# Kernel tuning notes

Measured on AMD Instinct MI355X. Metric: run time of the kernel, lower is better.

Reference implementation:

```python
import jax, jax.numpy as jnp
import numpy as np
import math

DIM = 1024
N_HEADS = 16
HEAD_DIM = DIM // N_HEADS
MAX_SEQ_LEN = 2048


def rope_tables(seq_len, head_dim):
    inv_freq = 1.0 / (10000.0 ** (jnp.arange(0, head_dim, 2, dtype=jnp.float32) / head_dim))
    t = jnp.arange(seq_len, dtype=jnp.float32)
    freqs = jnp.einsum('i,j->ij', t, inv_freq)          # [T, D/2]
    emb = jnp.concatenate([freqs, freqs], axis=-1)      # [T, D]
    return jnp.cos(emb), jnp.sin(emb)


def rotate_half(x):
    x1, x2 = jnp.split(x, 2, axis=-1)
    return jnp.concatenate([-x2, x1], axis=-1)


def setup_inputs() -> dict:
    key = jax.random.key(0)
    k1, k2, k3 = jax.random.split(key, 3)
    B, T = 4, 2048
    x = jax.random.normal(k1, (B, T, DIM), dtype=jnp.float32)
    # Linear(dim, 3*dim, bias=False) and Linear(dim, dim, bias=False); stored as [in, out]
    Wqkv = jax.random.normal(k2, (DIM, 3 * DIM), dtype=jnp.float32) * (1.0 / math.sqrt(DIM))
    Wproj = jax.random.normal(k3, (DIM, DIM), dtype=jnp.float32) * (1.0 / math.sqrt(DIM))
    return {"x": x, "Wqkv": Wqkv, "Wproj": Wproj}


def reference(x, Wqkv, Wproj):
    B, T, C = x.shape
    qkv = x @ Wqkv                                       # [B,T,3C]
    q, k, v = jnp.split(qkv, 3, axis=-1)
    # [B,T,C] -> [B,H,T,D]
    def to_heads(t_):
        return t_.reshape(B, T, N_HEADS, HEAD_DIM).transpose(0, 2, 1, 3)
    q, k, v = to_heads(q), to_heads(k), to_heads(v)
    cos, sin = rope_tables(T, HEAD_DIM)                  # [T,D]
    cos = cos[None, None, :, :]
    sin = sin[None, None, :, :]
    q = q * cos + rotate_half(q) * sin
    k = k * cos + rotate_half(k) * sin
    scale = 1.0 / math.sqrt(HEAD_DIM)
    att = jnp.einsum('bhqd,bhkd->bhqk', q, k) * scale    # [B,H,T,T]
    causal = jnp.triu(jnp.ones((T, T), dtype=bool), k=1)
    att = jnp.where(causal[None, None], -jnp.inf, att)
    att = jax.nn.softmax(att, axis=-1)
    y = jnp.einsum('bhqk,bhkd->bhqd', att, v)            # [B,H,T,D]
    y = y.transpose(0, 2, 1, 3).reshape(B, T, C)
    return y @ Wproj
```

## Files before the change

### kernel.cpp

```cpp
#include <hip/hip_runtime.h>
#include <hip/hip_bf16.h>

typedef unsigned short u16;
typedef __attribute__((ext_vector_type(8))) short short8;
typedef __attribute__((ext_vector_type(4))) float floatx4;

__device__ __forceinline__ u16 f2bf(float f) {
    union { float f; unsigned u; } v; v.f = f;
    unsigned r = v.u + 0x7fffu + ((v.u >> 16) & 1u);
    return (u16)(r >> 16);
}
__device__ __forceinline__ float fexp2(float x) {
#if __has_builtin(__builtin_amdgcn_exp2f)
    return __builtin_amdgcn_exp2f(x);
#else
    return exp2f(x);
#endif
}
__device__ __forceinline__ unsigned cvtpk_bf16(float lo, float hi) {
    unsigned r;
    asm("v_cvt_pk_bf16_f32 %0, %1, %2" : "=v"(r) : "v"(lo), "v"(hi));
    return r;
}
__device__ __forceinline__ void permlane32_swap(unsigned &a, unsigned &b) {
    asm("v_permlane32_swap_b32 %0, %1" : "+v"(a), "+v"(b));
}
__device__ __forceinline__ void permlane16_swap(unsigned &a, unsigned &b) {
    asm("v_permlane16_swap_b32 %0, %1" : "+v"(a), "+v"(b));
}

__device__ __forceinline__ void async_load16(const void* g, void* l) {
    __builtin_amdgcn_global_load_lds(
        (const __attribute__((address_space(1))) unsigned int*)g,
        (__attribute__((address_space(3))) unsigned int*)l, 16, 0, 0);
}

#define B_   4
#define T_   2048
#define NH_  16
#define HD_  64
#define DIM_ 1024
#define M_   (B_ * T_)
#define NQKV (3 * DIM_)
#define NT_  16
#define LOG2E 1.4426950408889634f

__global__ __launch_bounds__(256) void preproc(const float* __restrict__ x,
                                               const float* __restrict__ Wqkv,
                                               const float* __restrict__ Wproj,
                                               u16* __restrict__ xb,
                                               u16* __restrict__ wqt,
                                               u16* __restrict__ wpt,
                                               float* __restrict__ tabc,
                                               float* __restrict__ tabs) {
    __shared__ float tile[32][33];
    const int bid = blockIdx.x, tid = threadIdx.x;
    if (bid < 8192) {
        int idx = bid * 256 + tid;
        float4 v = ((const float4*)x)[idx];
        ushort4 o;
        o.x = f2bf(v.x); o.y = f2bf(v.y); o.z = f2bf(v.z); o.w = f2bf(v.w);
        ((ushort4*)xb)[idx] = o;
    } else if (bid < 12288) {
        const float* in; u16* outp; int Cn, bx, by;
        if (bid < 11264) { int blk = bid - 8192;  in = Wqkv;  outp = wqt; Cn = NQKV; bx = blk % 96; by = blk / 96; }
        else             { int blk = bid - 11264; in = Wproj; outp = wpt; Cn = DIM_; bx = blk & 31; by = blk >> 5; }
        const int R = DIM_;
        int c0 = bx * 32, r0 = by * 32;
        int tx = tid & 31, ty = tid >> 5;
#pragma unroll
        for (int i = 0; i < 4; ++i)
            tile[ty + i * 8][tx] = in[(size_t)(r0 + ty + i * 8) * Cn + c0 + tx];
        __syncthreads();
#pragma unroll
        for (int i = 0; i < 4; ++i)
            outp[(size_t)(c0 + ty + i * 8) * R + r0 + tx] = f2bf(tile[tx][ty + i * 8]);
    } else {
        int idx = (bid - 12288) * 256 + tid;
        int t = idx >> 5, j = idx & 31;
        double invf = pow(10000.0, -(double)j / 32.0);
        double th = (double)t * invf;
        tabc[idx] = (float)cos(th);
        tabs[idx] = (float)sin(th);
    }
}

__device__ __forceinline__ void gemm_core(const u16* __restrict__ A,
                                          const u16* __restrict__ Bt,
                                          u16* smem, int m0, int n0, int tid,
                                          floatx4 (&acc)[2][4]) {
    const int wave = tid >> 6, lane = tid & 63;
    const int ln15 = lane & 15, quad = lane >> 4;
    const int wm = (wave & 3) * 32, wn = (wave >> 2) * 64;
    const int l8 = lane & 7, ld8 = lane >> 3;
    const int sgc = (l8 ^ ld8) * 8;
    const int K = DIM_;

    const u16* aS = A + (size_t)(m0 + wave * 8 + ld8) * K + sgc;
    const u16* bS = Bt + (size_t)(n0 + wave * 16 + ld8) * K + sgc;

    auto issue3 = [&](int k2, u16* As2, u16* Bs2) {
        async_load16(aS + k2,          As2 + (wave * 8) * 64);
        async_load16(bS + k2,          Bs2 + (wave * 16) * 64);
        async_load16(bS + 8 * K + k2,  Bs2 + (wave * 16 + 8) * 64);
    };
    auto compute = [&](const u16* As_c, const u16* Bs_c, int c4) {
        short8 af[2], bfv[4];
#pragma unroll
        for (int i = 0; i < 2; ++i) {
            int row = wm + i * 16 + ln15;
            af[i] = *(const short8*)&As_c[row * 64 + (((c4 + quad) ^ (row & 7)) << 3)];
        }
#pragma unroll
        for (int j = 0; j < 4; ++j) {
            int row = wn + j * 16 + ln15;
            bfv[j] = *(const short8*)&Bs_c[row * 64 + (((c4 + quad) ^ (row & 7)) << 3)];
        }
        __builtin_amdgcn_s_setprio(1);
#pragma unroll
        for (int i = 0; i < 2; ++i)
#pragma unroll
            for (int j = 0; j < 4; ++j)
                acc[i][j] = __builtin_amdgcn_mfma_f32_16x16x32_bf16(
                    af[i], bfv[j], acc[i][j], 0, 0, 0);
        __builtin_amdgcn_s_setprio(0);
    };

    issue3(0, smem, smem + 24576);
    issue3(64, smem + 8192, smem + 24576 + 16384);

#pragma unroll 1
    for (int t = 0; t < NT_; ++t) {
        if (t < NT_ - 1) asm volatile("s_waitcnt vmcnt(3)" ::: "memory");
        else             asm volatile("s_waitcnt vmcnt(0)" ::: "memory");
        __builtin_amdgcn_s_barrier();
        asm volatile("" ::: "memory");

        const int cb = t % 3, cb2 = (t + 2) % 3;
        const u16* As_c = smem + cb * 8192;
        const u16* Bs_c = smem + 24576 + cb * 16384;
        u16* As2 = smem + cb2 * 8192;
        u16* Bs2 = smem + 24576 + cb2 * 16384;

        if (t < NT_ - 2) issue3((t + 2) * 64, As2, Bs2);
        compute(As_c, Bs_c, 0);
        compute(As_c, Bs_c, 4);
        asm volatile("" ::: "memory");
    }
}

__global__ __launch_bounds__(1024, 4) void gemm_qkv(const u16* __restrict__ A,
                                                    const u16* __restrict__ Bt,
                                                    const float* __restrict__ tabc,
                                                    const float* __restrict__ tabs,
                                                    u16* __restrict__ Qo,
                                                    u16* __restrict__ Ko,
                                                    u16* __restrict__ Vt) {
    __shared__ __align__(16) u16 smem[73728];
    const int tid = threadIdx.x;
    const int bid = blockIdx.x;
    const int wg = (bid & 7) * 96 + (bid >> 3);
    const int bx = wg / 64, by = wg - bx * 64;
    const int m0 = by * 128, n0 = bx * 256;

    floatx4 acc[2][4] = {};
    gemm_core(A, Bt, smem, m0, n0, tid, acc);

    const int wave = tid >> 6, lane = tid & 63;
    const int ln15 = lane & 15, quad = lane >> 4;
    const int wm = (wave & 3) * 32, wn = (wave >> 2) * 64;

    __syncthreads();
    u16* Es = smem;
    const int sel = n0 >> 10;
    auto es_put = [&](int row, int col, u16 v) {
        int c = col >> 3;
        int pc = (c & 24) | ((c & 7) ^ (row & 7));
        Es[row * 256 + pc * 8 + (col & 7)] = v;
    };
    if (sel == 2) {
#pragma unroll
        for (int i = 0; i < 2; ++i)
#pragma unroll
            for (int j = 0; j < 4; ++j)
#pragma unroll
                for (int r = 0; r < 4; ++r)
                    es_put(wm + i * 16 + quad * 4 + r, wn + j * 16 + ln15,
                           f2bf(acc[i][j][r]));
    } else {
        const float scale = sel ? 1.0f : 0.125f * LOG2E;
#pragma unroll
        for (int i = 0; i < 2; ++i)
#pragma unroll
            for (int jjl = 0; jjl < 2; ++jjl) {
                int j = jjl * 16 + ln15;
#pragma unroll
                for (int r = 0; r < 4; ++r) {
                    int row = wm + i * 16 + quad * 4 + r;
                    int t = (m0 + row) & (T_ - 1);
                    float cs = tabc[t * 32 + j], sn = tabs[t * 32 + j];
                    float xl = acc[i][jjl][r], xh = acc[i][jjl + 2][r];
                    es_put(row, wn + j,      f2bf((xl * cs - xh * sn) * scale));
                    es_put(row, wn + j + 32, f2bf((xh * cs + xl * sn) * scale));
                }
            }
    }
    __syncthreads();
    if (sel == 2) {
        const int bq = m0 >> 11;
        const int t0 = m0 & (T_ - 1);
        const int h0 = (n0 & 1023) >> 6;
#pragma unroll
        for (int a = 0; a < 2; ++a) {
            int aid = tid + a * 1024;
            int hh = aid >> 9;
            int rem = aid & 511;
            int tseg = rem >> 5;
            int d2 = rem & 31;
            int col = hh * 64 + 2 * d2;
            int cch = col >> 3;
            u16 lo8[8], hi8[8];
#pragma unroll
            for (int j = 0; j < 8; ++j) {
                int row = tseg * 8 + j;
                int pc = (cch & 24) | ((cch & 7) ^ (row & 7));
                unsigned w = *(const unsigned*)&Es[row * 256 + pc * 8 + (col & 7)];
                lo8[j] = (u16)(w & 0xffffu);
                hi8[j] = (u16)(w >> 16);
            }
            size_t ob = ((size_t)((bq * NH_ + h0 + hh) * HD_) + 2 * d2) * T_ + t0 + tseg * 8;
            *(uint4*)(Vt + ob) = *(const uint4*)lo8;
            *(uint4*)(Vt + ob + T_) = *(const uint4*)hi8;
        }
    } else {
        const int bb = m0 >> 11;
        u16* outqk = (sel == 1) ? Ko : Qo;
#pragma unroll
        for (int k = 0; k < 4; ++k) {
            int cid = tid + k * 1024;
            int row = cid >> 5, c = cid & 31;
            int pc = (c & 24) | ((c & 7) ^ (row & 7));
            uint4 v = *(const uint4*)&Es[row * 256 + pc * 8];
            int h = ((n0 & 1023) >> 6) + (c >> 3);
            int d = (c & 7) * 8;
            int t = (m0 + row) & (T_ - 1);
            *(uint4*)&outqk[((size_t)(bb * NH_ + h) * T_ + t) * HD_ + d] = v;
        }
    }
}

__device__ __forceinline__ void gemm_core128(const u16* __restrict__ A,
                                             const u16* __restrict__ Bt,
                                             u16* smem, int m0, int n0, int tid,
                                             floatx4 (&acc)[4][4]) {
    const int wave = tid >> 6, lane = tid & 63;
    const int ln15 = lane & 15, quad = lane >> 4;
    const int wm = (wave & 1) * 64, wn = (wave >> 1) * 64;
    const int l8 = lane & 7, ld8 = lane >> 3;
    const int sgc = (l8 ^ ld8) * 8;
    const int K = DIM_;

    const u16* aS = A + (size_t)(m0 + wave * 32 + ld8) * K + sgc;
    const u16* bS = Bt + (size_t)(n0 + wave * 32 + ld8) * K + sgc;

    auto stage = [&](int k0, u16* buf) {
#pragma unroll
        for (int it = 0; it < 4; ++it) {
            async_load16(aS + (size_t)(it * 8) * K + k0,
                         buf + (wave * 32 + it * 8) * 64);
            async_load16(bS + (size_t)(it * 8) * K + k0,
                         buf + 8192 + (wave * 32 + it * 8) * 64);
        }
    };
    auto compute = [&](const u16* buf, int c4) {
        short8 af[4], bfv[4];
#pragma unroll
        for (int i = 0; i < 4; ++i) {
            int row = wm + i * 16 + ln15;
            af[i] = *(const short8*)&buf[row * 64 + (((c4 + quad) ^ (row & 7)) << 3)];
        }
#pragma unroll
        for (int j = 0; j < 4; ++j) {
            int row = wn + j * 16 + ln15;
            bfv[j] = *(const short8*)&buf[8192 + row * 64 + (((c4 + quad) ^ (row & 7)) << 3)];
        }
        __builtin_amdgcn_s_setprio(1);
#pragma unroll
        for (int i = 0; i < 4; ++i)
#pragma unroll
            for (int j = 0; j < 4; ++j)
                acc[i][j] = __builtin_amdgcn_mfma_f32_16x16x32_bf16(
                    af[i], bfv[j], acc[i][j], 0, 0, 0);
        __builtin_amdgcn_s_setprio(0);
    };

    stage(0, smem);
#pragma unroll 1
    for (int t = 0; t < NT_; ++t) {
        asm volatile("s_waitcnt vmcnt(0)" ::: "memory");
        __builtin_amdgcn_s_barrier();
        asm volatile("" ::: "memory");
        if (t + 1 < NT_) stage((t + 1) * 64, smem + ((t + 1) & 1) * 16384);
        const u16* cur = smem + (t & 1) * 16384;
        compute(cur, 0);
        compute(cur, 4);
        asm volatile("" ::: "memory");
    }
}

__global__ __launch_bounds__(256, 4) void gemm_proj(const u16* __restrict__ A,
                                                    const u16* __restrict__ Bt,
                                                    float* __restrict__ C) {
    __shared__ __align__(16) u16 smem[32768];
    const int tid = threadIdx.x;
    const int bid = blockIdx.x;
    const int local = bid >> 3;
    const int by = (bid & 7) * 8 + (local & 7);
    const int bx = local >> 3;
    const int m0 = by * 128, n0 = bx * 128;

    floatx4 acc[4][4] = {};
    gemm_core128(A, Bt, smem, m0, n0, tid, acc);

    const int wave = tid >> 6, lane = tid & 63;
    const int ln15 = lane & 15, quad = lane >> 4;
    const int wm = (wave & 1) * 64, wn = (wave >> 1) * 64;
#pragma unroll
    for (int i = 0; i < 4; ++i)
#pragma unroll
        for (int jj = 0; jj < 4; ++jj)
#pragma unroll
            for (int r = 0; r < 4; ++r) {
                int m = m0 + wm + i * 16 + quad * 4 + r;
                int n = n0 + wn + jj * 16 + ln15;
                C[(size_t)m * DIM_ + n] = acc[i][jj][r];
            }
}

__global__ __launch_bounds__(256, 5) void attn_kernel(const u16* __restrict__ Q,
                                                      const u16* __restrict__ Kh,
                                                      const u16* __restrict__ Vt,
                                                      u16* __restrict__ Y) {
    __shared__ __align__(16) u16 Kl[2][64 * 64];
    __shared__ __align__(16) u16 Vl[2][64 * 64];
    const int tid = threadIdx.x, wave = tid >> 6, lane = tid & 63;
    const int ln15 = lane & 15, quad = lane >> 4;
    const int bid = blockIdx.x;
    const int tidx = 31 - (bid >> 6);
    const int bh = bid & 63;
    const int b = bh >> 4, h = bh & 15;
    const int l8 = lane & 7, ld8 = lane >> 3;
    const int sgc = l8 ^ ld8;

    const u16* kbase = Kh + (size_t)bh * T_ * HD_;
    const u16* vbase = Vt + (size_t)bh * HD_ * T_;
    const short8 ones = {0x3F80, 0x3F80, 0x3F80, 0x3F80,
                         0x3F80, 0x3F80, 0x3F80, 0x3F80};
    const int srow = wave * 16;

    const int q0 = tidx * 64;
    const int bm = q0 + srow;

    const u16* qp = Q + ((size_t)bh * T_ + bm + ln15) * HD_;
    short8 qf0 = *(const short8*)(qp + quad * 8);
    short8 qf1 = *(const short8*)(qp + 32 + quad * 8);

    floatx4 o[5] = {};

#pragma unroll
    for (int it = 0; it < 2; ++it) {
        int r = srow + it * 8;
        async_load16(kbase + (size_t)(r + ld8) * HD_ + sgc * 8, &Kl[0][r * 64]);
        async_load16(vbase + (size_t)(r + ld8) * T_ + sgc * 8, &Vl[0][r * 64]);
    }

    for (int kt = 0; kt <= tidx; ++kt) {
        const int cur = kt & 1;
        __syncthreads();
        if (kt < tidx) {
            const int kn = (kt + 1) * 64;
#pragma unroll
            for (int it = 0; it < 2; ++it) {
                int r = srow + it * 8;
                async_load16(kbase + (size_t)(kn + r + ld8) * HD_ + sgc * 8,
                             &Kl[cur ^ 1][r * 64]);
                async_load16(vbase + (size_t)(r + ld8) * T_ + kn + sgc * 8,
                             &Vl[cur ^ 1][r * 64]);
            }
        }
        floatx4 s[4] = {};
        __builtin_amdgcn_s_setprio(1);
#pragma unroll
        for (int nt = 0; nt < 4; ++nt) {
            int row = nt * 16 + ln15;
            short8 kf0 = *(const short8*)&Kl[cur][row * 64 + ((quad ^ (row & 7)) << 3)];
            short8 kf1 = *(const short8*)&Kl[cur][row * 64 + (((4 + quad) ^ (row & 7)) << 3)];
            s[nt] = __builtin_amdgcn_mfma_f32_16x16x32_bf16(kf0, qf0, s[nt], 0, 0, 0);
            s[nt] = __builtin_amdgcn_mfma_f32_16x16x32_bf16(kf1, qf1, s[nt], 0, 0, 0);
        }
        __builtin_amdgcn_s_setprio(0);
        if (kt == tidx) {
            const int lim = srow + ln15;
#pragma unroll
            for (int nt = 0; nt < 4; ++nt) {
                int key = nt * 16 + quad * 4;
#pragma unroll
                for (int r = 0; r < 4; ++r)
                    s[nt][r] = (key + r > lim) ? 0.f : fexp2(s[nt][r]);
            }
        } else {
#pragma unroll
            for (int nt = 0; nt < 4; ++nt)
#pragma unroll
                for (int r = 0; r < 4; ++r) s[nt][r] = fexp2(s[nt][r]);
        }
        unsigned x0 = cvtpk_bf16(s[0][0], s[0][1]);
        unsigned x1 = cvtpk_bf16(s[1][0], s[1][1]);
        unsigned y0 = cvtpk_bf16(s[0][2], s[0][3]);
        unsigned y1 = cvtpk_bf16(s[1][2], s[1][3]);
        unsigned x2 = cvtpk_bf16(s[2][0], s[2][1]);
        unsigned x3 = cvtpk_bf16(s[3][0], s[3][1]);
        unsigned y2 = cvtpk_bf16(s[2][2], s[2][3]);
        unsigned y3 = cvtpk_bf16(s[3][2], s[3][3]);
        permlane32_swap(x0, x1); permlane16_swap(x0, x1);
        permlane32_swap(y0, y1); permlane16_swap(y0, y1);
        permlane32_swap(x2, x3); permlane16_swap(x2, x3);
        permlane32_swap(y2, y3); permlane16_swap(y2, y3);
        union { unsigned u[4]; short8 s8; } pk0, pk1;
        pk0.u[0] = x0; pk0.u[1] = y0; pk0.u[2] = x1; pk0.u[3] = y1;
        pk1.u[0] = x2; pk1.u[1] = y2; pk1.u[2] = x3; pk1.u[3] = y3;
        __builtin_amdgcn_s_setprio(1);
#pragma unroll
        for (int nt = 0; nt < 4; ++nt) {
            int row = nt * 16 + ln15;
            short8 vf0 = *(const short8*)&Vl[cur][row * 64 + ((quad ^ (row & 7)) << 3)];
            short8 vf1 = *(const short8*)&Vl[cur][row * 64 + (((4 + quad) ^ (row & 7)) << 3)];
            o[nt] = __builtin_amdgcn_mfma_f32_16x16x32_bf16(pk0.s8, vf0, o[nt], 0, 0, 0);
            o[nt] = __builtin_amdgcn_mfma_f32_16x16x32_bf16(pk1.s8, vf1, o[nt], 0, 0, 0);
        }
        o[4] = __builtin_amdgcn_mfma_f32_16x16x32_bf16(pk0.s8, ones, o[4], 0, 0, 0);
        o[4] = __builtin_amdgcn_mfma_f32_16x16x32_bf16(pk1.s8, ones, o[4], 0, 0, 0);
        __builtin_amdgcn_s_setprio(0);
    }
#pragma unroll
    for (int r = 0; r < 4; ++r) {
        float inv = 1.f / o[4][r];
        int row = bm + quad * 4 + r;
        u16* yp = Y + ((size_t)(b * T_ + row)) * DIM_ + h * HD_;
#pragma unroll
        for (int nt = 0; nt < 4; ++nt)
            yp[nt * 16 + ln15] = f2bf(o[nt][r] * inv);
    }
}

extern "C" void kernel_launch(void* const* d_in, const int* in_sizes, int n_in,
                              void* d_out, int out_size, void* d_ws, size_t ws_size,
                              hipStream_t stream) {
    const float* x     = (const float*)d_in[0];
    const float* Wqkv  = (const float*)d_in[1];
    const float* Wproj = (const float*)d_in[2];
    float* out = (float*)d_out;
    char* ws = (char*)d_ws;

    const size_t SZ_XB  = (size_t)M_ * DIM_ * 2;
    const size_t SZ_WQT = (size_t)NQKV * DIM_ * 2;
    const size_t SZ_WPT = (size_t)DIM_ * DIM_ * 2;
    const size_t SZ_Q   = SZ_XB;
    const size_t SZ_TAB = (size_t)T_ * 32 * 4;

    u16*   xb   = (u16*)(ws);
    u16*   wqt  = (u16*)(ws + SZ_XB);
    u16*   wpt  = (u16*)(ws + SZ_XB + SZ_WQT);
    u16*   qb   = (u16*)(ws + SZ_XB + SZ_WQT + SZ_WPT);
    u16*   kb   = (u16*)(ws + SZ_XB + SZ_WQT + SZ_WPT + SZ_Q);
    u16*   vtb  = (u16*)(ws + SZ_XB + SZ_WQT + SZ_WPT + 3 * SZ_Q);
    float* tabc = (float*)(ws + SZ_XB + SZ_WQT + SZ_WPT + 4 * SZ_Q);
    float* tabs = (float*)(ws + SZ_XB + SZ_WQT + SZ_WPT + 4 * SZ_Q + SZ_TAB);
    u16*   yb   = xb;

    preproc<<<12544, 256, 0, stream>>>(x, Wqkv, Wproj, xb, wqt, wpt, tabc, tabs);
    gemm_qkv<<<768, 1024, 0, stream>>>(xb, wqt, tabc, tabs, qb, kb, vtb);
    attn_kernel<<<2048, 256, 0, stream>>>(qb, kb, vtb, yb);
    gemm_proj<<<512, 256, 0, stream>>>(yb, wpt, out);
}
```

Before: 236.8 us.

## Enlarge attention blocks to 256 queries with 16 waves sharing K/V tiles

The attention kernel now launches 512 blocks of 1024 threads, each covering 256 query rows with 16 waves instead of 64 rows with 4 waves. Each staged K/V tile is reused by four times as many waves, which cuts global and LDS staging traffic per query. The block schedule pairs reversed and forward tile orders for load balance. Waves whose rows lie entirely before a key tile skip compute but still take part in every barrier, so causal imbalance within a block costs idle waves and occupancy drops to two blocks per CU.

After: 245.1 us. 3.5% more time.

```diff
diff --git a/kernel.cpp b/kernel.cpp
--- a/kernel.cpp
+++ b/kernel.cpp
@@ -337,16 +337,16 @@
             }
 }
 
-__global__ __launch_bounds__(256, 5) void attn_kernel(const u16* __restrict__ Q,
-                                                      const u16* __restrict__ Kh,
-                                                      const u16* __restrict__ Vt,
-                                                      u16* __restrict__ Y) {
+__global__ __launch_bounds__(1024, 2) void attn_kernel(const u16* __restrict__ Q,
+                                                       const u16* __restrict__ Kh,
+                                                       const u16* __restrict__ Vt,
+                                                       u16* __restrict__ Y) {
     __shared__ __align__(16) u16 Kl[2][64 * 64];
     __shared__ __align__(16) u16 Vl[2][64 * 64];
     const int tid = threadIdx.x, wave = tid >> 6, lane = tid & 63;
     const int ln15 = lane & 15, quad = lane >> 4;
     const int bid = blockIdx.x;
-    const int tidx = 31 - (bid >> 6);
+    const int mt = (bid < 256) ? (7 - (bid >> 6)) : ((bid - 256) >> 6);
     const int bh = bid & 63;
     const int b = bh >> 4, h = bh & 15;
     const int l8 = lane & 7, ld8 = lane >> 3;
@@ -356,10 +356,18 @@
     const u16* vbase = Vt + (size_t)bh * HD_ * T_;
     const short8 ones = {0x3F80, 0x3F80, 0x3F80, 0x3F80,
                          0x3F80, 0x3F80, 0x3F80, 0x3F80};
-    const int srow = wave * 16;
-
-    const int q0 = tidx * 64;
-    const int bm = q0 + srow;
+
+    const int bm = mt * 256 + wave * 16;
+    const int w7 = wave & 7;
+    auto stage = [&](int kt, int buf) {
+        int r = w7 * 8 + ld8;
+        if (wave < 8)
+            async_load16(kbase + (size_t)(kt * 64 + r) * HD_ + sgc * 8,
+                         &Kl[buf][w7 * 8 * 64]);
+        else
+            async_load16(vbase + (size_t)r * T_ + kt * 64 + sgc * 8,
+                         &Vl[buf][w7 * 8 * 64]);
+    };
 
     const u16* qp = Q + ((size_t)bh * T_ + bm + ln15) * HD_;
     short8 qf0 = *(const short8*)(qp + quad * 8);
@@ -367,80 +375,70 @@
 
     floatx4 o[5] = {};
 
-#pragma unroll
-    for (int it = 0; it < 2; ++it) {
-        int r = srow + it * 8;
-        async_load16(kbase + (size_t)(r + ld8) * HD_ + sgc * 8, &Kl[0][r * 64]);
-        async_load16(vbase + (size_t)(r + ld8) * T_ + sgc * 8, &Vl[0][r * 64]);
-    }
-
-    for (int kt = 0; kt <= tidx; ++kt) {
+    stage(0, 0);
+
+    const int NKT = mt * 4 + 3;
+    for (int kt = 0; kt <= NKT; ++kt) {
         const int cur = kt & 1;
         __syncthreads();
-        if (kt < tidx) {
-            const int kn = (kt + 1) * 64;
-#pragma unroll
-            for (int it = 0; it < 2; ++it) {
-                int r = srow + it * 8;
-                async_load16(kbase + (size_t)(kn + r + ld8) * HD_ + sgc * 8,
-                             &Kl[cur ^ 1][r * 64]);
-                async_load16(vbase + (size_t)(r + ld8) * T_ + kn + sgc * 8,
-                             &Vl[cur ^ 1][r * 64]);
-            }
-        }
-        floatx4 s[4] = {};
-        __builtin_amdgcn_s_setprio(1);
-#pragma unroll
-        for (int nt = 0; nt < 4; ++nt) {
-            int row = nt * 16 + ln15;
-            short8 kf0 = *(const short8*)&Kl[cur][row * 64 + ((quad ^ (row & 7)) << 3)];
-            short8 kf1 = *(const short8*)&Kl[cur][row * 64 + (((4 + quad) ^ (row & 7)) << 3)];
-            s[nt] = __builtin_amdgcn_mfma_f32_16x16x32_bf16(kf0, qf0, s[nt], 0, 0, 0);
-            s[nt] = __builtin_amdgcn_mfma_f32_16x16x32_bf16(kf1, qf1, s[nt], 0, 0, 0);
-        }
-        __builtin_amdgcn_s_setprio(0);
-        if (kt == tidx) {
-            const int lim = srow + ln15;
+        if (kt < NKT) stage(kt + 1, cur ^ 1);
+
+        const int kb0 = kt * 64;
+        if (kb0 <= bm + 15) {
+            floatx4 s[4] = {};
+            __builtin_amdgcn_s_setprio(1);
 #pragma unroll
             for (int nt = 0; nt < 4; ++nt) {
-                int key = nt * 16 + quad * 4;
-#pragma unroll
-                for (int r = 0; r < 4; ++r)
-                    s[nt][r] = (key + r > lim) ? 0.f : fexp2(s[nt][r]);
-            }
-        } else {
-#pragma unroll
-            for (int nt = 0; nt < 4; ++nt)
-#pragma unroll
-                for (int r = 0; r < 4; ++r) s[nt][r] = fexp2(s[nt][r]);
-        }
-        unsigned x0 = cvtpk_bf16(s[0][0], s[0][1]);
-        unsigned x1 = cvtpk_bf16(s[1][0], s[1][1]);
-        unsigned y0 = cvtpk_bf16(s[0][2], s[0][3]);
-        unsigned y1 = cvtpk_bf16(s[1][2], s[1][3]);
-        unsigned x2 = cvtpk_bf16(s[2][0], s[2][1]);
-        unsigned x3 = cvtpk_bf16(s[3][0], s[3][1]);
-        unsigned y2 = cvtpk_bf16(s[2][2], s[2][3]);
-        unsigned y3 = cvtpk_bf16(s[3][2], s[3][3]);
-        permlane32_swap(x0, x1); permlane16_swap(x0, x1);
-        permlane32_swap(y0, y1); permlane16_swap(y0, y1);
-        permlane32_swap(x2, x3); permlane16_swap(x2, x3);
-        permlane32_swap(y2, y3); permlane16_swap(y2, y3);
-        union { unsigned u[4]; short8 s8; } pk0, pk1;
-        pk0.u[0] = x0; pk0.u[1] = y0; pk0.u[2] = x1; pk0.u[3] = y1;
-        pk1.u[0] = x2; pk1.u[1] = y2; pk1.u[2] = x3; pk1.u[3] = y3;
-        __builtin_amdgcn_s_setprio(1);
-#pragma unroll
-        for (int nt = 0; nt < 4; ++nt) {
-            int row = nt * 16 + ln15;
-            short8 vf0 = *(const short8*)&Vl[cur][row * 64 + ((quad ^ (row & 7)) << 3)];
-            short8 vf1 = *(const short8*)&Vl[cur][row * 64 + (((4 + quad) ^ (row & 7)) << 3)];
-            o[nt] = __builtin_amdgcn_mfma_f32_16x16x32_bf16(pk0.s8, vf0, o[nt], 0, 0, 0);
-            o[nt] = __builtin_amdgcn_mfma_f32_16x16x32_bf16(pk1.s8, vf1, o[nt], 0, 0, 0);
-        }
-        o[4] = __builtin_amdgcn_mfma_f32_16x16x32_bf16(pk0.s8, ones, o[4], 0, 0, 0);
-        o[4] = __builtin_amdgcn_mfma_f32_16x16x32_bf16(pk1.s8, ones, o[4], 0, 0, 0);
-        __builtin_amdgcn_s_setprio(0);
+                int row = nt * 16 + ln15;
+                short8 kf0 = *(const short8*)&Kl[cur][row * 64 + ((quad ^ (row & 7)) << 3)];
+                short8 kf1 = *(const short8*)&Kl[cur][row * 64 + (((4 + quad) ^ (row & 7)) << 3)];
+                s[nt] = __builtin_amdgcn_mfma_f32_16x16x32_bf16(kf0, qf0, s[nt], 0, 0, 0);
+                s[nt] = __builtin_amdgcn_mfma_f32_16x16x32_bf16(kf1, qf1, s[nt], 0, 0, 0);
+            }
+            __builtin_amdgcn_s_setprio(0);
+            if (kb0 + 63 > bm) {
+                const int lim = bm + ln15 - kb0;
+#pragma unroll
+                for (int nt = 0; nt < 4; ++nt) {
+                    int key = nt * 16 + quad * 4;
+#pragma unroll
+                    for (int r = 0; r < 4; ++r)
+                        s[nt][r] = (key + r > lim) ? 0.f : fexp2(s[nt][r]);
+                }
+            } else {
+#pragma unroll
+                for (int nt = 0; nt < 4; ++nt)
+#pragma unroll
+                    for (int r = 0; r < 4; ++r) s[nt][r] = fexp2(s[nt][r]);
+            }
+            unsigned x0 = cvtpk_bf16(s[0][0], s[0][1]);
+            unsigned x1 = cvtpk_bf16(s[1][0], s[1][1]);
+            unsigned y0 = cvtpk_bf16(s[0][2], s[0][3]);
+            unsigned y1 = cvtpk_bf16(s[1][2], s[1][3]);
+            unsigned x2 = cvtpk_bf16(s[2][0], s[2][1]);
+            unsigned x3 = cvtpk_bf16(s[3][0], s[3][1]);
+            unsigned y2 = cvtpk_bf16(s[2][2], s[2][3]);
+            unsigned y3 = cvtpk_bf16(s[3][2], s[3][3]);
+            permlane32_swap(x0, x1); permlane16_swap(x0, x1);
+            permlane32_swap(y0, y1); permlane16_swap(y0, y1);
+            permlane32_swap(x2, x3); permlane16_swap(x2, x3);
+            permlane32_swap(y2, y3); permlane16_swap(y2, y3);
+            union { unsigned u[4]; short8 s8; } pk0, pk1;
+            pk0.u[0] = x0; pk0.u[1] = y0; pk0.u[2] = x1; pk0.u[3] = y1;
+            pk1.u[0] = x2; pk1.u[1] = y2; pk1.u[2] = x3; pk1.u[3] = y3;
+            __builtin_amdgcn_s_setprio(1);
+#pragma unroll
+            for (int nt = 0; nt < 4; ++nt) {
+                int row = nt * 16 + ln15;
+                short8 vf0 = *(const short8*)&Vl[cur][row * 64 + ((quad ^ (row & 7)) << 3)];
+                short8 vf1 = *(const short8*)&Vl[cur][row * 64 + (((4 + quad) ^ (row & 7)) << 3)];
+                o[nt] = __builtin_amdgcn_mfma_f32_16x16x32_bf16(pk0.s8, vf0, o[nt], 0, 0, 0);
+                o[nt] = __builtin_amdgcn_mfma_f32_16x16x32_bf16(pk1.s8, vf1, o[nt], 0, 0, 0);
+            }
+            o[4] = __builtin_amdgcn_mfma_f32_16x16x32_bf16(pk0.s8, ones, o[4], 0, 0, 0);
+            o[4] = __builtin_amdgcn_mfma_f32_16x16x32_bf16(pk1.s8, ones, o[4], 0, 0, 0);
+            __builtin_amdgcn_s_setprio(0);
+        }
     }
 #pragma unroll
     for (int r = 0; r < 4; ++r) {
@@ -480,6 +478,6 @@
 
     preproc<<<12544, 256, 0, stream>>>(x, Wqkv, Wproj, xb, wqt, wpt, tabc, tabs);
     gemm_qkv<<<768, 1024, 0, stream>>>(xb, wqt, tabc, tabs, qb, kb, vtb);
-    attn_kernel<<<2048, 256, 0, stream>>>(qb, kb, vtb, yb);
+    attn_kernel<<<512, 1024, 0, stream>>>(qb, kb, vtb, yb);
     gemm_proj<<<512, 256, 0, stream>>>(yb, wpt, out);
 }
```
